# Kernel tuning notes

Hardware: AMD Instinct MI355X
Metric: run time of the kernel (lower is better)

The kernel has to match this reference:

```python
import jax, jax.numpy as jnp
import numpy as np

NOISE_EPS = 1e-2   # Shazeer noisy-gating stddev floor
LN_EPS = 1e-6
LOSS_COEF = 0.01
K = 2              # num_activated_experts


def _layer_norm(x, w, b):
    mu = jnp.mean(x, axis=-1, keepdims=True)
    var = jnp.var(x, axis=-1, keepdims=True)
    return (x - mu) * jax.lax.rsqrt(var + LN_EPS) * w + b


def _cv_squared(v):
    return jnp.var(v) / (jnp.mean(v) ** 2 + 1e-10)


def _normal_cdf(z):
    return 0.5 * (1.0 + jax.scipy.special.erf(z / jnp.sqrt(jnp.asarray(2.0, z.dtype))))


def setup_inputs() -> dict:
    key = jax.random.key(0)
    ks = jax.random.split(key, 8)
    N, D, H, O, E = 8192, 512, 1024, 512, 8
    x = jax.random.normal(ks[0], (N, D), jnp.float32)
    x_offsets = jnp.sort(jax.random.randint(ks[1], (17,), 0, N)).astype(jnp.int64)
    noise = jax.random.normal(ks[2], (N, E), jnp.float32)
    s = 0.02
    return {
        "x": x,
        "x_offsets": x_offsets,
        "max_seq_len": 2048,
        "noise": noise,
        "norm_w": jnp.ones((D,), jnp.float32),
        "norm_bias": jnp.zeros((D,), jnp.float32),
        "w_gate": jax.random.normal(ks[3], (D, E), jnp.float32) * s,
        "w_noise": jax.random.normal(ks[4], (D, E), jnp.float32) * s,
        "W1": jax.random.normal(ks[5], (E, H, D), jnp.float32) * s,  # [E, model_d, input]
        "b1": jnp.zeros((E, H), jnp.float32),
        "W2": jax.random.normal(ks[6], (E, O, H), jnp.float32) * s,  # [E, output, model_d]
        "b2": jnp.zeros((E, O), jnp.float32),
        "output_weight": jax.random.normal(ks[7], (D, O), jnp.float32) * s,
    }


def reference(x, x_offsets, max_seq_len, noise, norm_w, norm_bias, w_gate, w_noise,
              W1, b1, W2, b2, output_weight):
    N, D = x.shape
    E = w_gate.shape[1]
    k_plus = min(K + 1, E)

    # pre-norm
    x_norm = _layer_norm(x, norm_w, norm_bias)

    # noisy top-k gating (training path)
    clean_logits = x_norm @ w_gate                      # [N, E]
    noise_stddev = jax.nn.softplus(x_norm @ w_noise) + NOISE_EPS
    noisy_logits = clean_logits + noise * noise_stddev

    top_logits, top_indices = jax.lax.top_k(noisy_logits, k_plus)   # [N, k+1]
    top_k_logits = top_logits[:, :K]
    top_k_indices = top_indices[:, :K]
    top_k_gates = jax.nn.softmax(top_k_logits, axis=-1)             # [N, K]

    rows = jnp.arange(N)[:, None]
    gates = jnp.zeros((N, E), top_k_gates.dtype).at[rows, top_k_indices].set(top_k_gates)

    # load = prob each expert is in top-k under the gating noise (Shazeer)
    flat = top_logits.reshape(-1)
    pos_in = jnp.arange(N) * k_plus + K
    thr_in = flat[pos_in][:, None]          # (k+1)-th value: threshold if already in
    thr_out = flat[pos_in - 1][:, None]     # k-th value: threshold if currently out
    is_in = noisy_logits > thr_in
    prob_in = _normal_cdf((clean_logits - thr_in) / noise_stddev)
    prob_out = _normal_cdf((clean_logits - thr_out) / noise_stddev)
    load_probs = jnp.where(is_in, prob_in, prob_out)                # [N, E]

    loss = LOSS_COEF * (_cv_squared(gates.sum(0)) + _cv_squared(load_probs.sum(0)))

    # dispatch stats: tokens per expert
    lengths = jnp.zeros((E,), jnp.float32).at[top_k_indices.reshape(-1)].add(1.0)
    load = lengths / lengths.sum()

    # grouped expert MLP (dense one-hot combine; gates are 0 for unrouted experts)
    h = jnp.einsum('nd,ehd->neh', x_norm, W1) + b1                  # [N, E, H]
    a = jax.nn.silu(h)
    y_e = jnp.einsum('neh,eoh->neo', a, W2) + b2                    # [N, E, O]
    y_moe = jnp.einsum('ne,neo->no', gates, y_e)                    # [N, O]

    # shared expert: addmm(y, shared_x=x, output_weight)
    y = y_moe + x @ output_weight
    return y, loss, load
```

## Files before the change

### kernel.cpp

```cpp
#include <hip/hip_runtime.h>
#include <math.h>

typedef unsigned short u16;
typedef unsigned int u32;

#define N_ROWS 8192
#define DDIM 512
#define HDIM 1024
#define ODIM 512
#define NEXP 8
#define MAXPAIRS (N_ROWS * 2)
#define MAXPOS (MAXPAIRS + NEXP * 128)
#define MAXTILES (MAXPOS / 128)

#define SM_CNT 0
#define SM_CUR 8
#define SM_AOFF 16
#define SM_GSUM 32
#define SM_LSUM 40
#define SM_WORDS 64

using short8 = __attribute__((ext_vector_type(8))) short;
using float4v = __attribute__((ext_vector_type(4))) float;

__device__ __forceinline__ u16 f2bf(float f) {
    union { float f; u32 u; } v; v.f = f;
    u32 u = v.u;
    return (u16)((u + 0x7fffu + ((u >> 16) & 1u)) >> 16);
}

__device__ __forceinline__ void async_copy16(u16* lds, const u16* g) {
    __builtin_amdgcn_global_load_lds(
        (const __attribute__((address_space(1))) void*)g,
        (__attribute__((address_space(3))) void*)lds, 16, 0, 0);
}

__global__ __launch_bounds__(512) void init1_kernel(int* small, float* zeropage) {
    int i = threadIdx.x;
    if (i < SM_WORDS) small[i] = 0;
    zeropage[i] = 0.f;
}

#define CONV_BLOCKS 8192
#define GATE_BLOCKS 512
__global__ __launch_bounds__(256) void combo_kernel(
    const float* __restrict__ x, const float* __restrict__ noise,
    const float* __restrict__ norm_w, const float* __restrict__ norm_b,
    const float* __restrict__ w_gate, const float* __restrict__ w_noise,
    const float* __restrict__ W1, const float* __restrict__ W2, const float* __restrict__ ow,
    u16* __restrict__ xnorm_bf, u16* __restrict__ x_bf,
    int* __restrict__ pair_expert, float* __restrict__ pair_gate,
    u16* __restrict__ W1b, u16* __restrict__ W2b, u16* __restrict__ owT,
    int* __restrict__ small, int* __restrict__ bucket_rows)
{
    __shared__ __align__(16) float sh[NEXP * DDIM * 2 + 64];
    int b = blockIdx.x, tid = threadIdx.x;

    if (b >= GATE_BLOCKS) {
        int cb = b - GATE_BLOCKS;
        if (cb < CONV_BLOCKS) {
            const size_t n4 = (size_t)NEXP * HDIM * DDIM / 4;
            size_t i = (size_t)cb * 256 + tid;
            const float* src; u16* dst;
            if (i < n4) { src = W1; dst = W1b; } else { src = W2; dst = W2b; i -= n4; }
            float4 v = ((const float4*)src)[i];
            ushort4 o;
            o.x = f2bf(v.x); o.y = f2bf(v.y); o.z = f2bf(v.z); o.w = f2bf(v.w);
            ((ushort4*)dst)[i] = o;
        } else if (cb < CONV_BLOCKS + 256) {
            float (*tile)[33] = (float(*)[33])sh;
            int t = cb - CONV_BLOCKS;
            int bx = (t & 15) * 32, by = (t >> 4) * 32;
            int tx = tid & 31, ty = tid >> 5;
            for (int r = ty; r < 32; r += 8) tile[r][tx] = ow[(size_t)(by + r) * ODIM + bx + tx];
            __syncthreads();
            for (int r = ty; r < 32; r += 8) owT[(size_t)(bx + r) * DDIM + by + tx] = f2bf(tile[tx][r]);
        } else {
            int i = (cb - CONV_BLOCKS - 256) * 256 + tid;
            if (i < MAXPOS) bucket_rows[i] = -1;
        }
        return;
    }

    float* wgT = sh;
    float* wnT = sh + NEXP * DDIM;
    float* blk_g = sh + 2 * NEXP * DDIM;
    float* blk_l = blk_g + NEXP;
    int* blk_c = (int*)(blk_l + NEXP);
    float* smf = (float*)small;

    for (int i = tid; i < NEXP * DDIM; i += 256) {
        int d = i >> 3, e = i & 7;
        wgT[e * DDIM + d] = w_gate[i];
        wnT[e * DDIM + d] = w_noise[i];
    }
    if (tid < NEXP) { blk_g[tid] = 0.f; blk_l[tid] = 0.f; blk_c[tid] = 0; }
    __syncthreads();

    int wave = tid >> 6, lane = tid & 63;
    float nw[8], nb[8];
#pragma unroll
    for (int j = 0; j < 8; j++) { nw[j] = norm_w[j * 64 + lane]; nb[j] = norm_b[j * 64 + lane]; }

    for (int r = 0; r < 4; ++r) {
        int row = b * 16 + wave * 4 + r;
        const float* xr = x + (size_t)row * DDIM;
        float xv[8], s = 0.f, s2 = 0.f;
#pragma unroll
        for (int j = 0; j < 8; j++) { float v = xr[j * 64 + lane]; xv[j] = v; s += v; s2 += v * v; }
#pragma unroll
        for (int o = 32; o; o >>= 1) { s += __shfl_xor(s, o, 64); s2 += __shfl_xor(s2, o, 64); }
        float mu = s * (1.f / DDIM);
        float var = s2 * (1.f / DDIM) - mu * mu;
        float rstd = rsqrtf(var + 1e-6f);

        float acc[16];
#pragma unroll
        for (int e = 0; e < 16; e++) acc[e] = 0.f;
#pragma unroll
        for (int j = 0; j < 8; j++) {
            float v = (xv[j] - mu) * rstd * nw[j] + nb[j];
            int d = j * 64 + lane;
            xnorm_bf[(size_t)row * DDIM + d] = f2bf(v);
            x_bf[(size_t)row * DDIM + d] = f2bf(xv[j]);
#pragma unroll
            for (int e = 0; e < 8; e++) {
                acc[e] += v * wgT[e * DDIM + d];
                acc[8 + e] += v * wnT[e * DDIM + d];
            }
        }
#pragma unroll
        for (int e = 0; e < 16; e++)
#pragma unroll
            for (int o = 32; o; o >>= 1) acc[e] += __shfl_xor(acc[e], o, 64);

        float cl[8], sd[8], nz[8];
#pragma unroll
        for (int e = 0; e < 8; e++) {
            cl[e] = acc[e];
            float t = acc[8 + e];
            float sp = fmaxf(t, 0.f) + log1pf(expf(-fabsf(t)));
            sd[e] = sp + 0.01f;
            nz[e] = cl[e] + noise[(size_t)row * NEXP + e] * sd[e];
        }
        int idx[3]; float val[3]; u32 msk = 0;
#pragma unroll
        for (int t = 0; t < 3; t++) {
            float best = -INFINITY; int bi = 0;
#pragma unroll
            for (int e = 0; e < 8; e++)
                if (!((msk >> e) & 1) && nz[e] > best) { best = nz[e]; bi = e; }
            idx[t] = bi; val[t] = best; msk |= 1u << bi;
        }
        float e1 = expf(val[1] - val[0]);
        float g0 = 1.f / (1.f + e1), g1 = e1 / (1.f + e1);
        float thr_in = val[2], thr_out = val[1];

        if (lane == 0) {
            pair_expert[row * 2] = idx[0]; pair_gate[row * 2] = g0;
            pair_expert[row * 2 + 1] = idx[1]; pair_gate[row * 2 + 1] = g1;
            atomicAdd(&blk_g[idx[0]], g0); atomicAdd(&blk_g[idx[1]], g1);
            atomicAdd(&blk_c[idx[0]], 1); atomicAdd(&blk_c[idx[1]], 1);
#pragma unroll
            for (int e = 0; e < 8; e++) {
                float thr = (nz[e] > thr_in) ? thr_in : thr_out;
                float z = (cl[e] - thr) / sd[e];
                float p = 0.5f * (1.f + erff(z * 0.70710678118654752f));
                atomicAdd(&blk_l[e], p);
            }
        }
    }
    __syncthreads();
    if (tid < NEXP) {
        atomicAdd(smf + SM_GSUM + tid, blk_g[tid]);
        atomicAdd(smf + SM_LSUM + tid, blk_l[tid]);
        atomicAdd(&small[SM_CNT + tid], blk_c[tid]);
    }
}

__global__ __launch_bounds__(256) void scatter_kernel(
    const int* __restrict__ pair_expert, const float* __restrict__ pair_gate,
    int* __restrict__ small, int* __restrict__ bucket_rows, float* __restrict__ gate_by_pos,
    float* __restrict__ out_loss, float* __restrict__ out_load)
{
    __shared__ int aoff[NEXP + 1];
    __shared__ int blk_cnt[NEXP];
    __shared__ int blk_base[NEXP];
    int tid = threadIdx.x;
    if (tid == 0) {
        int acc = 0; aoff[0] = 0;
        for (int e = 0; e < NEXP; e++) { acc += (small[SM_CNT + e] + 127) & ~127; aoff[e + 1] = acc; }
    }
    if (tid < NEXP) blk_cnt[tid] = 0;
    __syncthreads();
    int p = blockIdx.x * 256 + tid;
    int e = pair_expert[p];
    int local = atomicAdd(&blk_cnt[e], 1);
    __syncthreads();
    if (tid < NEXP)
        blk_base[tid] = aoff[tid] + atomicAdd(&small[SM_CUR + tid], blk_cnt[tid]);
    if (blockIdx.x == 0 && tid < NEXP + 1) small[SM_AOFF + tid] = aoff[tid];
    __syncthreads();
    int pos = blk_base[e] + local;
    bucket_rows[pos] = p >> 1;
    gate_by_pos[pos] = pair_gate[p];

    if (blockIdx.x == 0 && tid == 0) {
        const float* gs = (const float*)small + SM_GSUM;
        const float* ls = (const float*)small + SM_LSUM;
        float cv[2];
        for (int t = 0; t < 2; t++) {
            const float* v = t ? ls : gs;
            float m = 0.f;
            for (int k = 0; k < NEXP; k++) m += v[k];
            m *= (1.f / NEXP);
            float var = 0.f;
            for (int k = 0; k < NEXP; k++) { float d = v[k] - m; var += d * d; }
            var *= (1.f / NEXP);
            cv[t] = var / (m * m + 1e-10f);
        }
        out_loss[0] = 0.01f * (cv[0] + cv[1]);
        int tot = 0;
        for (int k = 0; k < NEXP; k++) tot += small[SM_CNT + k];
        float inv = 1.f / (float)tot;
        for (int k = 0; k < NEXP; k++) out_load[k] = (float)small[SM_CNT + k] * inv;
    }
}


__global__ __launch_bounds__(256) void gemmA_kernel(
    const u16* __restrict__ xnorm, const u16* __restrict__ xbf,
    const u16* __restrict__ W1b, const u16* __restrict__ owT,
    const int* __restrict__ bucket_rows, const int* __restrict__ small,
    const float* __restrict__ b1, const u16* __restrict__ zeropage,
    u16* __restrict__ a_buf, float* __restrict__ y)
{
    constexpr int KD = 512;
    __shared__ __align__(16) u16 As[128 * 64];
    __shared__ __align__(16) u16 Bs[128 * 64];

    int tid = threadIdx.x;
    bool m0 = blockIdx.y < 8;
    int base, bn, e = 0;
    const u16* Bsel;
    if (m0) {
        base = blockIdx.x * 128;
        if (base >= small[SM_AOFF + 8]) return;
        while (e < 7 && base >= small[SM_AOFF + e + 1]) ++e;
        bn = blockIdx.y * 128;
        Bsel = W1b + (size_t)e * HDIM * KD;
    } else {
        int j = (blockIdx.y - 8) * 136 + blockIdx.x;
        if (j >= 256) return;
        base = (j >> 2) * 128;
        bn = (j & 3) * 128;
        Bsel = owT;
    }

    int wave = tid >> 6, lane = tid & 63;
    int lr = lane >> 3;
    int lc = ((lane & 7) ^ lr) * 8;

    const u16* ga[4]; const u16* gb[4];
    u16* la[4]; u16* lb[4];
#pragma unroll
    for (int c = 0; c < 4; c++) {
        int tr = wave * 32 + c * 8;
        if (m0) {
            int r0 = bucket_rows[base + tr + lr];
            ga[c] = ((r0 < 0) ? zeropage : xnorm + (size_t)r0 * KD) + lc;
        } else {
            ga[c] = xbf + (size_t)(base + tr + lr) * KD + lc;
        }
        gb[c] = Bsel + (size_t)(bn + tr + lr) * KD + lc;
        la[c] = &As[tr * 64];
        lb[c] = &Bs[tr * 64];
    }

    int wm = (wave & 1) * 64, wn = (wave >> 1) * 64;
    int fr = lane & 15, kq = lane >> 4, f7 = fr & 7;

    float4v acc[4][4];
#pragma unroll
    for (int i = 0; i < 4; i++)
#pragma unroll
        for (int j = 0; j < 4; j++) acc[i][j] = (float4v){0.f, 0.f, 0.f, 0.f};

    for (int k0 = 0; k0 < KD; k0 += 64) {
        __syncthreads();
#pragma unroll
        for (int c = 0; c < 4; c++) async_copy16(la[c], ga[c] + k0);
#pragma unroll
        for (int c = 0; c < 4; c++) async_copy16(lb[c], gb[c] + k0);
        __syncthreads();
        short8 af[4][2], bf[4][2];
#pragma unroll
        for (int mt = 0; mt < 4; mt++)
#pragma unroll
            for (int kh = 0; kh < 2; kh++)
                af[mt][kh] = *(const short8*)&As[(wm + mt * 16 + fr) * 64 + (((kq + 4 * kh) ^ f7) * 8)];
#pragma unroll
        for (int nt = 0; nt < 4; nt++)
#pragma unroll
            for (int kh = 0; kh < 2; kh++)
                bf[nt][kh] = *(const short8*)&Bs[(wn + nt * 16 + fr) * 64 + (((kq + 4 * kh) ^ f7) * 8)];
#pragma unroll
        for (int mt = 0; mt < 4; mt++)
#pragma unroll
            for (int nt = 0; nt < 4; nt++) {
                acc[mt][nt] = __builtin_amdgcn_mfma_f32_16x16x32_bf16(af[mt][0], bf[nt][0], acc[mt][nt], 0, 0, 0);
                acc[mt][nt] = __builtin_amdgcn_mfma_f32_16x16x32_bf16(af[mt][1], bf[nt][1], acc[mt][nt], 0, 0, 0);
            }
    }

    int rbase = (lane >> 4) * 4, c16 = lane & 15;
#pragma unroll
    for (int nt = 0; nt < 4; nt++) {
        int gn = bn + wn + nt * 16 + c16;
        float bv = m0 ? b1[e * HDIM + gn] : 0.f;
#pragma unroll
        for (int mt = 0; mt < 4; mt++) {
            int gm = base + wm + mt * 16 + rbase;
#pragma unroll
            for (int r = 0; r < 4; r++) {
                float v = acc[mt][nt][r];
                if (m0) {
                    float h = v + bv;
                    float a = h * __builtin_amdgcn_rcpf(1.f + __expf(-h));
                    a_buf[(size_t)(gm + r) * HDIM + gn] = f2bf(a);
                } else {
                    y[(size_t)(gm + r) * ODIM + gn] = v;
                }
            }
        }
    }
}

__global__ __launch_bounds__(256) void gemmB_kernel(
    const u16* __restrict__ a_buf, const u16* __restrict__ W2b,
    const int* __restrict__ bucket_rows, const int* __restrict__ small,
    const float* __restrict__ b2, const float* __restrict__ gate_by_pos,
    float* __restrict__ y)
{
    constexpr int KD = 1024;
    __shared__ __align__(16) u16 As[128 * 64];
    __shared__ __align__(16) u16 Bs[128 * 64];

    int tid = threadIdx.x;
    int base = blockIdx.x * 128;
    if (base >= small[SM_AOFF + 8]) return;
    int e = 0;
    while (e < 7 && base >= small[SM_AOFF + e + 1]) ++e;
    int bn = blockIdx.y * 128;

    int wave = tid >> 6, lane = tid & 63;
    int lr = lane >> 3;
    int lc = ((lane & 7) ^ lr) * 8;

    const u16* Bsel = W2b + (size_t)e * ODIM * KD;
    const u16* ga[4]; const u16* gb[4];
    u16* la[4]; u16* lb[4];
#pragma unroll
    for (int c = 0; c < 4; c++) {
        int tr = wave * 32 + c * 8;
        ga[c] = a_buf + (size_t)(base + tr + lr) * KD + lc;
        gb[c] = Bsel + (size_t)(bn + tr + lr) * KD + lc;
        la[c] = &As[tr * 64];
        lb[c] = &Bs[tr * 64];
    }

    int wm = (wave & 1) * 64, wn = (wave >> 1) * 64;
    int fr = lane & 15, kq = lane >> 4, f7 = fr & 7;

    float4v acc[4][4];
#pragma unroll
    for (int i = 0; i < 4; i++)
#pragma unroll
        for (int j = 0; j < 4; j++) acc[i][j] = (float4v){0.f, 0.f, 0.f, 0.f};

    for (int k0 = 0; k0 < KD; k0 += 64) {
        __syncthreads();
#pragma unroll
        for (int c = 0; c < 4; c++) async_copy16(la[c], ga[c] + k0);
#pragma unroll
        for (int c = 0; c < 4; c++) async_copy16(lb[c], gb[c] + k0);
        __syncthreads();
        short8 af[4][2], bf[4][2];
#pragma unroll
        for (int mt = 0; mt < 4; mt++)
#pragma unroll
            for (int kh = 0; kh < 2; kh++)
                af[mt][kh] = *(const short8*)&As[(wm + mt * 16 + fr) * 64 + (((kq + 4 * kh) ^ f7) * 8)];
#pragma unroll
        for (int nt = 0; nt < 4; nt++)
#pragma unroll
            for (int kh = 0; kh < 2; kh++)
                bf[nt][kh] = *(const short8*)&Bs[(wn + nt * 16 + fr) * 64 + (((kq + 4 * kh) ^ f7) * 8)];
#pragma unroll
        for (int mt = 0; mt < 4; mt++)
#pragma unroll
            for (int nt = 0; nt < 4; nt++) {
                acc[mt][nt] = __builtin_amdgcn_mfma_f32_16x16x32_bf16(af[mt][0], bf[nt][0], acc[mt][nt], 0, 0, 0);
                acc[mt][nt] = __builtin_amdgcn_mfma_f32_16x16x32_bf16(af[mt][1], bf[nt][1], acc[mt][nt], 0, 0, 0);
            }
    }

    int rbase = (lane >> 4) * 4, c16 = lane & 15;
#pragma unroll
    for (int mt = 0; mt < 4; mt++) {
        int pos0 = base + wm + mt * 16 + rbase;
        int rows[4]; float gs[4];
#pragma unroll
        for (int r = 0; r < 4; r++) { rows[r] = bucket_rows[pos0 + r]; gs[r] = gate_by_pos[pos0 + r]; }
#pragma unroll
        for (int nt = 0; nt < 4; nt++) {
            int gn = bn + wn + nt * 16 + c16;
            float b2v = b2[e * ODIM + gn];
#pragma unroll
            for (int r = 0; r < 4; r++) {
                if (rows[r] >= 0)
                    unsafeAtomicAdd(&y[(size_t)rows[r] * ODIM + gn], gs[r] * (acc[mt][nt][r] + b2v));
            }
        }
    }
}

extern "C" void kernel_launch(void* const* d_in, const int* in_sizes, int n_in,
                              void* d_out, int out_size, void* d_ws, size_t ws_size,
                              hipStream_t stream)
{
    (void)in_sizes; (void)n_in; (void)out_size; (void)ws_size;
    const float* x = (const float*)d_in[0];
    const float* noise = (const float*)d_in[3];
    const float* norm_w = (const float*)d_in[4];
    const float* norm_b = (const float*)d_in[5];
    const float* w_gate = (const float*)d_in[6];
    const float* w_noise = (const float*)d_in[7];
    const float* W1 = (const float*)d_in[8];
    const float* b1 = (const float*)d_in[9];
    const float* W2 = (const float*)d_in[10];
    const float* b2 = (const float*)d_in[11];
    const float* ow = (const float*)d_in[12];

    float* y = (float*)d_out;
    float* out_loss = y + (size_t)N_ROWS * ODIM;
    float* out_load = out_loss + 1;

    char* ws = (char*)d_ws;
    size_t off = 0;
    auto alloc = [&](size_t b) { size_t p = off; off = (off + b + 255) & ~(size_t)255; return p; };
    u16* xnorm_bf = (u16*)(ws + alloc((size_t)N_ROWS * DDIM * 2));
    u16* x_bf     = (u16*)(ws + alloc((size_t)N_ROWS * DDIM * 2));
    u16* W1b      = (u16*)(ws + alloc((size_t)NEXP * HDIM * DDIM * 2));
    u16* W2b      = (u16*)(ws + alloc((size_t)NEXP * ODIM * HDIM * 2));
    u16* owT      = (u16*)(ws + alloc((size_t)DDIM * ODIM * 2));
    u16* a_buf    = (u16*)(ws + alloc((size_t)MAXPOS * HDIM * 2));
    int* pair_expert = (int*)(ws + alloc((size_t)MAXPAIRS * 4));
    float* pair_gate = (float*)(ws + alloc((size_t)MAXPAIRS * 4));
    float* gate_by_pos = (float*)(ws + alloc((size_t)MAXPOS * 4));
    int* bucket_rows = (int*)(ws + alloc((size_t)MAXPOS * 4));
    int* small       = (int*)(ws + alloc(SM_WORDS * 4));
    float* zeropage  = (float*)(ws + alloc(2048));

    init1_kernel<<<1, 512, 0, stream>>>(small, zeropage);
    combo_kernel<<<GATE_BLOCKS + CONV_BLOCKS + 256 + 68, 256, 0, stream>>>(
        x, noise, norm_w, norm_b, w_gate, w_noise, W1, W2, ow,
        xnorm_bf, x_bf, pair_expert, pair_gate, W1b, W2b, owT, small, bucket_rows);
    scatter_kernel<<<MAXPAIRS / 256, 256, 0, stream>>>(pair_expert, pair_gate, small,
                                                       bucket_rows, gate_by_pos, out_loss, out_load);
    gemmA_kernel<<<dim3(MAXTILES, 10), 256, 0, stream>>>(xnorm_bf, x_bf, W1b, owT, bucket_rows,
                                                         small, b1, (const u16*)zeropage, a_buf, y);
    gemmB_kernel<<<dim3(MAXTILES, ODIM / 128), 256, 0, stream>>>(a_buf, W2b, bucket_rows, small,
                                                                 b2, gate_by_pos, y);
}
```

Baseline: 279.5 us.

## Move W2 bf16 conversion into gemmA grid and shrink gemmB K-tile to 32

The W2 fp32-to-bf16 conversion leaves combo_kernel and runs as 16 extra grid rows appended to gemmA, so it overlaps with the first GEMM instead of lengthening the gating/conversion stage. gemmB now uses a K-step of 32 with a smaller, unswizzled LDS tile: one MFMA per fragment pair per step and four async copies per thread. The smaller tile lowers LDS use and may raise occupancy, but it doubles the number of barrier-synchronized iterations. Dropping the XOR swizzle may also bring back LDS bank conflicts.

```diff
diff --git a/kernel.cpp b/kernel.cpp
--- a/kernel.cpp
+++ b/kernel.cpp
@@ -41,16 +41,16 @@
     zeropage[i] = 0.f;
 }
 
-#define CONV_BLOCKS 8192
+#define W1CONV_BLOCKS 4096
 #define GATE_BLOCKS 512
 __global__ __launch_bounds__(256) void combo_kernel(
     const float* __restrict__ x, const float* __restrict__ noise,
     const float* __restrict__ norm_w, const float* __restrict__ norm_b,
     const float* __restrict__ w_gate, const float* __restrict__ w_noise,
-    const float* __restrict__ W1, const float* __restrict__ W2, const float* __restrict__ ow,
+    const float* __restrict__ W1, const float* __restrict__ ow,
     u16* __restrict__ xnorm_bf, u16* __restrict__ x_bf,
     int* __restrict__ pair_expert, float* __restrict__ pair_gate,
-    u16* __restrict__ W1b, u16* __restrict__ W2b, u16* __restrict__ owT,
+    u16* __restrict__ W1b, u16* __restrict__ owT,
     int* __restrict__ small, int* __restrict__ bucket_rows)
 {
     __shared__ __align__(16) float sh[NEXP * DDIM * 2 + 64];
@@ -58,25 +58,22 @@
 
     if (b >= GATE_BLOCKS) {
         int cb = b - GATE_BLOCKS;
-        if (cb < CONV_BLOCKS) {
-            const size_t n4 = (size_t)NEXP * HDIM * DDIM / 4;
+        if (cb < W1CONV_BLOCKS) {
             size_t i = (size_t)cb * 256 + tid;
-            const float* src; u16* dst;
-            if (i < n4) { src = W1; dst = W1b; } else { src = W2; dst = W2b; i -= n4; }
-            float4 v = ((const float4*)src)[i];
+            float4 v = ((const float4*)W1)[i];
             ushort4 o;
             o.x = f2bf(v.x); o.y = f2bf(v.y); o.z = f2bf(v.z); o.w = f2bf(v.w);
-            ((ushort4*)dst)[i] = o;
-        } else if (cb < CONV_BLOCKS + 256) {
+            ((ushort4*)W1b)[i] = o;
+        } else if (cb < W1CONV_BLOCKS + 256) {
             float (*tile)[33] = (float(*)[33])sh;
-            int t = cb - CONV_BLOCKS;
+            int t = cb - W1CONV_BLOCKS;
             int bx = (t & 15) * 32, by = (t >> 4) * 32;
             int tx = tid & 31, ty = tid >> 5;
             for (int r = ty; r < 32; r += 8) tile[r][tx] = ow[(size_t)(by + r) * ODIM + bx + tx];
             __syncthreads();
             for (int r = ty; r < 32; r += 8) owT[(size_t)(bx + r) * DDIM + by + tx] = f2bf(tile[tx][r]);
         } else {
-            int i = (cb - CONV_BLOCKS - 256) * 256 + tid;
+            int i = (cb - W1CONV_BLOCKS - 256) * 256 + tid;
             if (i < MAXPOS) bucket_rows[i] = -1;
         }
         return;
@@ -231,6 +228,7 @@
 __global__ __launch_bounds__(256) void gemmA_kernel(
     const u16* __restrict__ xnorm, const u16* __restrict__ xbf,
     const u16* __restrict__ W1b, const u16* __restrict__ owT,
+    const float* __restrict__ W2, u16* __restrict__ W2b,
     const int* __restrict__ bucket_rows, const int* __restrict__ small,
     const float* __restrict__ b1, const u16* __restrict__ zeropage,
     u16* __restrict__ a_buf, float* __restrict__ y)
@@ -240,6 +238,20 @@
     __shared__ __align__(16) u16 Bs[128 * 64];
 
     int tid = threadIdx.x;
+    if (blockIdx.y >= 10) {
+        int j = (blockIdx.y - 10) * 136 + blockIdx.x;
+        if (j >= 2048) return;
+        size_t i = (size_t)j * 512 + tid;
+#pragma unroll
+        for (int t = 0; t < 2; t++, i += 256) {
+            float4 v = ((const float4*)W2)[i];
+            ushort4 o;
+            o.x = f2bf(v.x); o.y = f2bf(v.y); o.z = f2bf(v.z); o.w = f2bf(v.w);
+            ((ushort4*)W2b)[i] = o;
+        }
+        return;
+    }
+
     bool m0 = blockIdx.y < 8;
     int base, bn, e = 0;
     const u16* Bsel;
@@ -343,8 +355,8 @@
     float* __restrict__ y)
 {
     constexpr int KD = 1024;
-    __shared__ __align__(16) u16 As[128 * 64];
-    __shared__ __align__(16) u16 Bs[128 * 64];
+    __shared__ __align__(16) u16 As[128 * 32];
+    __shared__ __align__(16) u16 Bs[128 * 32];
 
     int tid = threadIdx.x;
     int base = blockIdx.x * 128;
@@ -354,23 +366,20 @@
     int bn = blockIdx.y * 128;
 
     int wave = tid >> 6, lane = tid & 63;
-    int lr = lane >> 3;
-    int lc = ((lane & 7) ^ lr) * 8;
-
+    const int trow = wave * 32 + (lane >> 2);
+    const int kcol = (lane & 3) * 8;
+    const u16* ga0 = a_buf + (size_t)(base + trow) * KD + kcol;
+    const u16* ga1 = a_buf + (size_t)(base + trow + 16) * KD + kcol;
     const u16* Bsel = W2b + (size_t)e * ODIM * KD;
-    const u16* ga[4]; const u16* gb[4];
-    u16* la[4]; u16* lb[4];
-#pragma unroll
-    for (int c = 0; c < 4; c++) {
-        int tr = wave * 32 + c * 8;
-        ga[c] = a_buf + (size_t)(base + tr + lr) * KD + lc;
-        gb[c] = Bsel + (size_t)(bn + tr + lr) * KD + lc;
-        la[c] = &As[tr * 64];
-        lb[c] = &Bs[tr * 64];
-    }
+    const u16* gb0 = Bsel + (size_t)(bn + trow) * KD + kcol;
+    const u16* gb1 = Bsel + (size_t)(bn + trow + 16) * KD + kcol;
+    u16* lA0 = &As[(wave * 32) * 32];
+    u16* lA1 = &As[(wave * 32 + 16) * 32];
+    u16* lB0 = &Bs[(wave * 32) * 32];
+    u16* lB1 = &Bs[(wave * 32 + 16) * 32];
 
     int wm = (wave & 1) * 64, wn = (wave >> 1) * 64;
-    int fr = lane & 15, kq = lane >> 4, f7 = fr & 7;
+    int fr = lane & 15, kg = (lane >> 4) * 8;
 
     float4v acc[4][4];
 #pragma unroll
@@ -378,31 +387,23 @@
 #pragma unroll
         for (int j = 0; j < 4; j++) acc[i][j] = (float4v){0.f, 0.f, 0.f, 0.f};
 
-    for (int k0 = 0; k0 < KD; k0 += 64) {
+    for (int k0 = 0; k0 < KD; k0 += 32) {
         __syncthreads();
-#pragma unroll
-        for (int c = 0; c < 4; c++) async_copy16(la[c], ga[c] + k0);
-#pragma unroll
-        for (int c = 0; c < 4; c++) async_copy16(lb[c], gb[c] + k0);
+        async_copy16(lA0, ga0 + k0);
+        async_copy16(lA1, ga1 + k0);
+        async_copy16(lB0, gb0 + k0);
+        async_copy16(lB1, gb1 + k0);
         __syncthreads();
-        short8 af[4][2], bf[4][2];
+        short8 af[4], bf[4];
+#pragma unroll
+        for (int mt = 0; mt < 4; mt++) af[mt] = *(const short8*)&As[(wm + mt * 16 + fr) * 32 + kg];
+#pragma unroll
+        for (int nt = 0; nt < 4; nt++) bf[nt] = *(const short8*)&Bs[(wn + nt * 16 + fr) * 32 + kg];
 #pragma unroll
         for (int mt = 0; mt < 4; mt++)
 #pragma unroll
-            for (int kh = 0; kh < 2; kh++)
-                af[mt][kh] = *(const short8*)&As[(wm + mt * 16 + fr) * 64 + (((kq + 4 * kh) ^ f7) * 8)];
-#pragma unroll
-        for (int nt = 0; nt < 4; nt++)
-#pragma unroll
-            for (int kh = 0; kh < 2; kh++)
-                bf[nt][kh] = *(const short8*)&Bs[(wn + nt * 16 + fr) * 64 + (((kq + 4 * kh) ^ f7) * 8)];
-#pragma unroll
-        for (int mt = 0; mt < 4; mt++)
-#pragma unroll
-            for (int nt = 0; nt < 4; nt++) {
-                acc[mt][nt] = __builtin_amdgcn_mfma_f32_16x16x32_bf16(af[mt][0], bf[nt][0], acc[mt][nt], 0, 0, 0);
-                acc[mt][nt] = __builtin_amdgcn_mfma_f32_16x16x32_bf16(af[mt][1], bf[nt][1], acc[mt][nt], 0, 0, 0);
-            }
+            for (int nt = 0; nt < 4; nt++)
+                acc[mt][nt] = __builtin_amdgcn_mfma_f32_16x16x32_bf16(af[mt], bf[nt], acc[mt][nt], 0, 0, 0);
     }
 
     int rbase = (lane >> 4) * 4, c16 = lane & 15;
@@ -463,13 +464,14 @@
     float* zeropage  = (float*)(ws + alloc(2048));
 
     init1_kernel<<<1, 512, 0, stream>>>(small, zeropage);
-    combo_kernel<<<GATE_BLOCKS + CONV_BLOCKS + 256 + 68, 256, 0, stream>>>(
-        x, noise, norm_w, norm_b, w_gate, w_noise, W1, W2, ow,
-        xnorm_bf, x_bf, pair_expert, pair_gate, W1b, W2b, owT, small, bucket_rows);
+    combo_kernel<<<GATE_BLOCKS + W1CONV_BLOCKS + 256 + 68, 256, 0, stream>>>(
+        x, noise, norm_w, norm_b, w_gate, w_noise, W1, ow,
+        xnorm_bf, x_bf, pair_expert, pair_gate, W1b, owT, small, bucket_rows);
     scatter_kernel<<<MAXPAIRS / 256, 256, 0, stream>>>(pair_expert, pair_gate, small,
                                                        bucket_rows, gate_by_pos, out_loss, out_load);
-    gemmA_kernel<<<dim3(MAXTILES, 10), 256, 0, stream>>>(xnorm_bf, x_bf, W1b, owT, bucket_rows,
-                                                         small, b1, (const u16*)zeropage, a_buf, y);
+    gemmA_kernel<<<dim3(MAXTILES, 10 + 16), 256, 0, stream>>>(xnorm_bf, x_bf, W1b, owT, W2, W2b,
+                                                              bucket_rows, small, b1,
+                                                              (const u16*)zeropage, a_buf, y);
     gemmB_kernel<<<dim3(MAXTILES, ODIM / 128), 256, 0, stream>>>(a_buf, W2b, bucket_rows, small,
                                                                  b2, gate_by_pos, y);
 }
```

Measured after the change: 256.2 us. 1.09x faster.
